# Optimization experiments

Hardware: AMD Instinct MI355X
Metric: run time of the kernel (lower is better)

Reference implementation:

```python
import jax, jax.numpy as jnp
import numpy as np

EMB_DIM = 1024
HEAD_NUM = 16
HEAD_DIM = EMB_DIM // HEAD_NUM
B, S = 2, 2048


def setup_inputs() -> dict:
    key = jax.random.key(0)
    k_x, k_wqkv, k_bqkv, k_wo, k_bo = jax.random.split(key, 5)
    x = jax.random.normal(k_x, (B, S, EMB_DIM), dtype=jnp.float32)
    # nn.Linear default init scale ~ 1/sqrt(fan_in); exact distribution irrelevant for a reference
    lim = 1.0 / np.sqrt(EMB_DIM)
    W_qkv = jax.random.uniform(k_wqkv, (EMB_DIM, 3 * EMB_DIM), jnp.float32, -lim, lim)
    b_qkv = jax.random.uniform(k_bqkv, (3 * EMB_DIM,), jnp.float32, -lim, lim)
    W_o = jax.random.uniform(k_wo, (EMB_DIM, EMB_DIM), jnp.float32, -lim, lim)
    b_o = jax.random.uniform(k_bo, (EMB_DIM,), jnp.float32, -lim, lim)
    mask = jnp.tril(jnp.ones((S, S), dtype=bool))  # causal mask as in casual_mask(seq_len)
    return {"x": x, "W_qkv": W_qkv, "b_qkv": b_qkv, "W_o": W_o, "b_o": b_o, "mask": mask}


def reference(x, W_qkv, b_qkv, W_o, b_o, mask):
    b, s, e = x.shape
    qkv = x @ W_qkv + b_qkv                      # [b, s, 3e]
    q, k, v = qkv[..., :e], qkv[..., e:2 * e], qkv[..., 2 * e:]
    # [b, s, h, d] -> [b, h, s, d]
    q = q.reshape(b, s, HEAD_NUM, HEAD_DIM).transpose(0, 2, 1, 3)
    k = k.reshape(b, s, HEAD_NUM, HEAD_DIM).transpose(0, 2, 1, 3)
    v = v.reshape(b, s, HEAD_NUM, HEAD_DIM).transpose(0, 2, 1, 3)
    scores = jnp.einsum("bhqd,bhkd->bhqk", q, k) / jnp.sqrt(jnp.float32(HEAD_DIM))
    scores = jnp.where(mask, scores, -jnp.inf)   # masked_fill(~mask, -inf)
    probs = jax.nn.softmax(scores, axis=-1)      # dropout is identity in eval mode
    out = jnp.einsum("bhqk,bhkd->bhqd", probs, v)
    out = out.transpose(0, 2, 1, 3).reshape(b, s, e)
    return out @ W_o + b_o
```

## Files before the change

### kernel.cpp

```cpp
#include <hip/hip_runtime.h>


typedef __attribute__((ext_vector_type(8))) short short8;
typedef __attribute__((ext_vector_type(4))) short short4v;
typedef __attribute__((ext_vector_type(4))) float floatx4;

#define NB 2
#define SEQ 2048
#define EMB 1024
#define NH 16
#define HD 64
#define M_ROWS (NB * SEQ)
#define N_QKV (3 * EMB)
#define SLOT_B 16896
#define SLOTS_PER_BH 24

#define GLL(g, l) __builtin_amdgcn_global_load_lds( \
    (const __attribute__((address_space(1))) void*)(g), \
    (__attribute__((address_space(3))) void*)(l), 16, 0, 0)

#if defined(__HIP_DEVICE_COMPILE__)
#define MFMA16K16(A, B, C) __builtin_amdgcn_mfma_f32_16x16x16bf16_1k(A, B, C, 0, 0, 0)
#else
#define MFMA16K16(A, B, C) (C)
#endif

static __device__ __forceinline__ unsigned short f2bf(float f) {
    union { float f; unsigned int u; } v; v.f = f;
    unsigned int r = v.u + 0x7FFFu + ((v.u >> 16) & 1u);
    return (unsigned short)(r >> 16);
}
static __device__ __forceinline__ float bf2f(unsigned short h) {
    union { unsigned int u; float f; } v; v.u = ((unsigned int)h) << 16;
    return v.f;
}

static __device__ __forceinline__ unsigned int cvt_pk_bf16(float lo, float hi) {
#if defined(__HIP_DEVICE_COMPILE__)
    unsigned int r;
    asm("v_cvt_pk_bf16_f32 %0, %1, %2" : "=v"(r) : "v"(lo), "v"(hi));
    return r;
#else
    (void)lo; (void)hi; return 0u;
#endif
}
static __device__ __forceinline__ short4v pack4bf(float a, float b, float c, float d) {
    union { unsigned int u[2]; short4v s; } pu;
    pu.u[0] = cvt_pk_bf16(a, b);
    pu.u[1] = cvt_pk_bf16(c, d);
    return pu.s;
}

__constant__ unsigned char FQT[40] = {
    3,11,14,15,15, 9,12,13,  7,11,14,15, 6, 9,12,13,
    7,11,15, 5, 6,10,13,14, 10, 2, 4, 5, 8,10,13,14,
    0, 1, 4, 8, 8, 9,12,12 };
__constant__ unsigned char FCI[40] = {
    0, 0, 1, 1, 3, 1, 1, 2,  0, 1, 3, 2, 0, 2, 3, 3,
    1, 2, 0, 0, 1, 0, 0, 0,  2, 0, 0, 1, 1, 1, 1, 2,
    0, 0, 1, 0, 2, 0, 0, 2 };

static __device__ __forceinline__ int slot_off(int qt2, int ci) {
    int so = (qt2 < 8) ? (qt2 - 4)
           : (qt2 < 12 ? 4 + (qt2 - 8) * 2 : 12 + (qt2 - 12) * 3);
    return so + (ci - 1);
}

__global__ void prep(const float* __restrict__ x,
                     const float* __restrict__ Wqkv, const float* __restrict__ Wo,
                     unsigned short* __restrict__ x_bf,
                     unsigned short* __restrict__ wqkvT, unsigned short* __restrict__ woT) {
    __shared__ unsigned short tile[32][33];
    int z = blockIdx.z;
    int tx = threadIdx.x, ty = threadIdx.y;
    if (z == 2) {
        int id = ((int)blockIdx.y * 96 + (int)blockIdx.x) * 256 + ty * 32 + tx;
        const int n4 = M_ROWS * EMB / 4;
        for (int i = id; i < n4; i += 96 * 32 * 256) {
            float4 v = ((const float4*)x)[i];
            unsigned long long p = (unsigned long long)f2bf(v.x)
                | ((unsigned long long)f2bf(v.y) << 16)
                | ((unsigned long long)f2bf(v.z) << 32)
                | ((unsigned long long)f2bf(v.w) << 48);
            ((unsigned long long*)x_bf)[i] = p;
        }
        return;
    }
    int C = z ? EMB : N_QKV;
    if ((int)blockIdx.x * 32 >= C) return;
    const float* in = z ? Wo : Wqkv;
    unsigned short* out = z ? woT : wqkvT;
    const int R = EMB;
    int c0 = blockIdx.x * 32, r0 = blockIdx.y * 32;
    #pragma unroll
    for (int j = 0; j < 4; ++j)
        tile[ty + j * 8][tx] = f2bf(in[(size_t)(r0 + ty + j * 8) * C + c0 + tx]);
    __syncthreads();
    #pragma unroll
    for (int j = 0; j < 4; ++j)
        out[(size_t)(c0 + ty + j * 8) * R + r0 + tx] = tile[tx][ty + j * 8];
}

#define CTS 130

__global__ __launch_bounds__(256) void qkv_gemm(
    const unsigned short* __restrict__ A,
    const unsigned short* __restrict__ Bt,
    const float* __restrict__ bias,
    unsigned short* __restrict__ qb, unsigned short* __restrict__ kb,
    unsigned short* __restrict__ vb)
{
    const int K = EMB;
    __shared__ __align__(16) unsigned short smem[128 * CTS];

    int t = threadIdx.x;
    int m0 = blockIdx.y * 128;
    int n0 = blockIdx.x * 128;
    int w = t >> 6, lane = t & 63, quad = lane >> 4, lcol = lane & 15;
    int wr = w >> 1, wc = w & 1;

    floatx4 zero = {0.f, 0.f, 0.f, 0.f};
    floatx4 acc[4][4];
    #pragma unroll
    for (int i = 0; i < 4; ++i)
        #pragma unroll
        for (int j = 0; j < 4; ++j) acc[i][j] = zero;

    const unsigned short* a0 = A  + (size_t)(m0 + (t >> 2)) * K + ((t & 3) << 3);
    const unsigned short* b0 = Bt + (size_t)(n0 + (t >> 2)) * K + ((t & 3) << 3);
    unsigned short* la = &smem[t << 3];

    GLL(a0, la);
    GLL(a0 + 64 * K, la + 2048);
    GLL(b0, la + 4096);
    GLL(b0 + 64 * K, la + 6144);

    for (int k0 = 0; k0 < K; k0 += 32) {
        int cur = (k0 >> 5) & 1, nxt = cur ^ 1;
        __syncthreads();
        if (k0 + 32 < K) {
            GLL(a0 + k0 + 32, la + nxt * 8192);
            GLL(a0 + 64 * K + k0 + 32, la + nxt * 8192 + 2048);
            GLL(b0 + k0 + 32, la + nxt * 8192 + 4096);
            GLL(b0 + 64 * K + k0 + 32, la + nxt * 8192 + 6144);
        }
        const unsigned short* As = &smem[cur * 8192];
        const unsigned short* Bs = As + 4096;
        short8 af[4], bfm[4];
        #pragma unroll
        for (int i = 0; i < 4; ++i)
            af[i] = *(const short8*)(&As[(wr * 64 + i * 16 + lcol) * 32 + quad * 8]);
        #pragma unroll
        for (int j = 0; j < 4; ++j)
            bfm[j] = *(const short8*)(&Bs[(wc * 64 + j * 16 + lcol) * 32 + quad * 8]);
        #pragma unroll
        for (int i = 0; i < 4; ++i)
            #pragma unroll
            for (int j = 0; j < 4; ++j)
                acc[i][j] = __builtin_amdgcn_mfma_f32_16x16x32_bf16(af[i], bfm[j], acc[i][j], 0, 0, 0);
    }

    bool isV = (n0 >= 2 * EMB);
    __syncthreads();
    #pragma unroll
    for (int i = 0; i < 4; ++i) {
        int row0 = wr * 64 + i * 16 + quad * 4;
        #pragma unroll
        for (int j = 0; j < 4; ++j) {
            int col = wc * 64 + j * 16 + lcol;
            float bv = bias[n0 + col];
            #pragma unroll
            for (int r = 0; r < 4; ++r) {
                unsigned short hv = f2bf(acc[i][j][r] + bv);
                if (isV) smem[col * CTS + row0 + r] = hv;
                else     smem[(row0 + r) * CTS + col] = hv;
            }
        }
    }
    __syncthreads();

    int b = m0 >> 11, s0 = m0 & 2047;
    int hbase = (n0 & 1023) >> 6;
    if (!isV) {
        unsigned short* dst = (n0 >= EMB) ? kb : qb;
        #pragma unroll
        for (int it = 0; it < 8; ++it) {
            int job = it * 32 + (t >> 3);
            int tok = job & 127, hh = job >> 7;
            int chunk = t & 7;
            short8 vv = *(const short8*)(&smem[tok * CTS + hh * 64 + chunk * 8]);
            size_t g = ((size_t)((b * NH + hbase + hh) * SEQ + s0 + tok)) * HD + chunk * 8;
            *(short8*)(&dst[g]) = vv;
        }
    } else {
        #pragma unroll
        for (int it = 0; it < 8; ++it) {
            int job = it * 32 + (t >> 3);
            int f = job & 127, half = job >> 7;
            int chunk = (t & 7) + half * 8;
            short8 vv = *(const short8*)(&smem[f * CTS + chunk * 8]);
            int h = hbase + (f >> 6), d = f & 63;
            size_t g = ((size_t)((b * NH + h) * HD + d)) * SEQ + s0 + chunk * 8;
            *(short8*)(&vb[g]) = vv;
        }
    }
}

__global__ __launch_bounds__(256) void attn_fused(
    const unsigned short* __restrict__ Q,
    const unsigned short* __restrict__ Kk,
    const unsigned short* __restrict__ Vt,
    unsigned short* __restrict__ Out,
    unsigned char* __restrict__ Part,
    float* __restrict__ Laux)
{
    __shared__ __align__(16) unsigned short Ks[2][64 * 64];
    __shared__ __align__(16) unsigned short Vs[2][64 * 64];

    int fid = (int)blockIdx.y * 40 + (int)blockIdx.x;
    int bh  = (fid & 7) * 4 + ((fid >> 3) & 3);
    int qq  = fid >> 5;
    int qt2 = FQT[qq];
    int ci  = FCI[qq];
    int nc  = 1 + (qt2 >> 2);
    int nt  = 2 * (qt2 + 1);
    int t0  = (nt * ci) / nc, t1 = (nt * (ci + 1)) / nc;
    int q0  = qt2 * 128;

    int t = threadIdx.x;
    int w = t >> 6, lane = t & 63, quad = lane >> 4, lcol = lane & 15;
    const size_t hoff = (size_t)bh * SEQ * HD;
    const float SC = 0.18033688011112043f;

    short8 aq[2][2];
    #pragma unroll
    for (int g = 0; g < 2; ++g) {
        const unsigned short* qp = Q + hoff
            + (size_t)(q0 + g * 64 + 16 * w + lcol) * HD + quad * 8;
        aq[g][0] = *(const short8*)qp;
        aq[g][1] = *(const short8*)(qp + 32);
    }

    int srow = t >> 3;
    int ss   = (t & 7) ^ (srow & 7);
    const unsigned short* kgl = Kk + hoff + (size_t)srow * HD + ss * 8;
    const unsigned short* vgl = Vt + hoff + (size_t)srow * SEQ + ss * 8;
    unsigned short* kld = &Ks[0][t * 8];
    unsigned short* vld = &Vs[0][t * 8];

    floatx4 zero = {0.f, 0.f, 0.f, 0.f};
    floatx4 O[2][4];
    floatx4 lacc[2];
    #pragma unroll
    for (int g = 0; g < 2; ++g) {
        lacc[g] = zero;
        #pragma unroll
        for (int td = 0; td < 4; ++td) O[g][td] = zero;
    }

    short4v ones4;
    #pragma unroll
    for (int jj = 0; jj < 4; ++jj) ones4[jj] = (short)0x3F80;

    {
        int pb = (t0 & 1) * 4096;
        size_t k0 = (size_t)t0 * 64;
        GLL(kgl + k0 * HD, kld + pb);
        GLL(kgl + (k0 + 32) * HD, kld + pb + 2048);
        GLL(vgl + k0, vld + pb);
        GLL(vgl + (size_t)32 * SEQ + k0, vld + pb + 2048);
    }

    int sx0 = (quad ^ (lcol & 7)) << 3;
    int sx1 = sx0 ^ 32;

    for (int kt = t0; kt < t1; ++kt) {
        int cur = kt & 1, nxt = cur ^ 1;
        __syncthreads();
        if (kt + 1 < t1) {
            size_t k0 = (size_t)(kt + 1) * 64;
            GLL(kgl + k0 * HD, kld + nxt * 4096);
            GLL(kgl + (k0 + 32) * HD, kld + nxt * 4096 + 2048);
            GLL(vgl + k0, vld + nxt * 4096);
            GLL(vgl + (size_t)32 * SEQ + k0, vld + nxt * 4096 + 2048);
        }

        const unsigned short* ksr = &Ks[cur][0];
        const unsigned short* vsr = &Vs[cur][0];
        short8 bk0[4], bk1[4];
        #pragma unroll
        for (int tc = 0; tc < 4; ++tc) {
            int rb = (tc * 16 + lcol) << 6;
            bk0[tc] = *(const short8*)(ksr + rb + sx0);
            bk1[tc] = *(const short8*)(ksr + rb + sx1);
        }

        short4v pk[2][4];
        bool act[2];
        #pragma unroll
        for (int g = 0; g < 2; ++g) {
            const int gb = q0 + g * 64 + 16 * w;
            act[g] = (kt * 64 <= gb + 15);
            if (act[g]) {
                floatx4 sacc[4];
                #pragma unroll
                for (int tc = 0; tc < 4; ++tc) {
                    sacc[tc] = __builtin_amdgcn_mfma_f32_16x16x32_bf16(bk0[tc], aq[g][0], zero, 0, 0, 0);
                    sacc[tc] = __builtin_amdgcn_mfma_f32_16x16x32_bf16(bk1[tc], aq[g][1], sacc[tc], 0, 0, 0);
                }
                if (kt * 64 + 63 > gb) {
                    int qrow = gb + lcol;
                    #pragma unroll
                    for (int tc = 0; tc < 4; ++tc) {
                        float p[4];
                        #pragma unroll
                        for (int r = 0; r < 4; ++r) {
                            float e = __builtin_amdgcn_exp2f(sacc[tc][r] * SC);
                            p[r] = (kt * 64 + tc * 16 + quad * 4 + r > qrow) ? 0.f : e;
                        }
                        pk[g][tc] = pack4bf(p[0], p[1], p[2], p[3]);
                    }
                } else {
                    #pragma unroll
                    for (int tc = 0; tc < 4; ++tc) {
                        pk[g][tc] = pack4bf(
                            __builtin_amdgcn_exp2f(sacc[tc][0] * SC),
                            __builtin_amdgcn_exp2f(sacc[tc][1] * SC),
                            __builtin_amdgcn_exp2f(sacc[tc][2] * SC),
                            __builtin_amdgcn_exp2f(sacc[tc][3] * SC));
                    }
                }
            }
        }

        #pragma unroll
        for (int td = 0; td < 4; ++td) {
            short4v va[4];
            #pragma unroll
            for (int tc = 0; tc < 4; ++tc) {
                int seg = ((tc << 1) + (quad >> 1)) ^ (lcol & 7);
                va[tc] = *(const short4v*)(vsr + ((td * 16 + lcol) << 6) + (seg << 3) + ((quad & 1) << 2));
            }
            if (act[0]) {
                #pragma unroll
                for (int tc = 0; tc < 4; ++tc)
                    O[0][td] = MFMA16K16(va[tc], pk[0][tc], O[0][td]);
            }
            if (act[1]) {
                #pragma unroll
                for (int tc = 0; tc < 4; ++tc)
                    O[1][td] = MFMA16K16(va[tc], pk[1][tc], O[1][td]);
            }
        }
        #pragma unroll
        for (int g = 0; g < 2; ++g) {
            if (act[g]) {
                #pragma unroll
                for (int tc = 0; tc < 4; ++tc)
                    lacc[g] = MFMA16K16(ones4, pk[g][tc], lacc[g]);
            }
        }
    }

    if (nc == 1) {
        int b = bh >> 4, h = bh & 15;
        #pragma unroll
        for (int g = 0; g < 2; ++g) {
            int qrow = q0 + g * 64 + 16 * w + lcol;
            float inv = 1.0f / lacc[g][0];
            size_t obase = ((size_t)b * SEQ + qrow) * EMB + (size_t)h * HD + quad * 4;
            #pragma unroll
            for (int td = 0; td < 4; ++td) {
                short4v ov;
                #pragma unroll
                for (int r = 0; r < 4; ++r) ov[r] = (short)f2bf(O[g][td][r] * inv);
                *(short4v*)(&Out[obase + td * 16]) = ov;
            }
        }
    } else if (ci == 0) {
        int b = bh >> 4, h = bh & 15;
        float* lrow = Laux + ((size_t)bh * 12 + (qt2 - 4)) * 128;
        #pragma unroll
        for (int g = 0; g < 2; ++g) {
            int ql = g * 64 + 16 * w + lcol;
            int qrow = q0 + ql;
            size_t obase = ((size_t)b * SEQ + qrow) * EMB + (size_t)h * HD + quad * 4;
            #pragma unroll
            for (int td = 0; td < 4; ++td) {
                short4v ov;
                #pragma unroll
                for (int r = 0; r < 4; ++r) ov[r] = (short)f2bf(O[g][td][r]);
                *(short4v*)(&Out[obase + td * 16]) = ov;
            }
            if (quad == 0) lrow[ql] = lacc[g][0];
        }
    } else {
        unsigned char* sp = Part
            + (size_t)(bh * SLOTS_PER_BH + slot_off(qt2, ci)) * SLOT_B;
        unsigned short* sO = (unsigned short*)sp;
        float* sL = (float*)(sp + 16384);
        #pragma unroll
        for (int g = 0; g < 2; ++g) {
            int ql = g * 64 + 16 * w + lcol;
            #pragma unroll
            for (int td = 0; td < 4; ++td) {
                short4v ov;
                #pragma unroll
                for (int r = 0; r < 4; ++r) ov[r] = (short)f2bf(O[g][td][r]);
                *(short4v*)(&sO[ql * 64 + td * 16 + quad * 4]) = ov;
            }
            if (quad == 0) sL[ql] = lacc[g][0];
        }
    }
}

__global__ __launch_bounds__(256) void attn_combine(
    const unsigned char* __restrict__ Part, const float* __restrict__ Laux,
    unsigned short* __restrict__ Out)
{
    int qt2 = 4 + (int)blockIdx.x;
    int bh = blockIdx.y;
    int nc = 1 + (qt2 >> 2);
    const unsigned char* base = Part
        + (size_t)(bh * SLOTS_PER_BH + slot_off(qt2, 1)) * SLOT_B;
    const float* lrow = Laux + ((size_t)bh * 12 + (qt2 - 4)) * 128;
    int b = bh >> 4, h = bh & 15;
    size_t obase = ((size_t)b * SEQ + qt2 * 128) * EMB + (size_t)h * HD;
    int t = threadIdx.x;
    #pragma unroll
    for (int it = 0; it < 4; ++it) {
        int job = it * 256 + t;
        int row = job >> 3, c8 = (job & 7) * 8;
        unsigned short* op = &Out[obase + (size_t)row * EMB + c8];
        float acc8[8];
        short8 v0 = *(const short8*)op;
        #pragma unroll
        for (int e = 0; e < 8; ++e) acc8[e] = bf2f((unsigned short)v0[e]);
        float lsum = lrow[row];
        for (int k = 1; k < nc; ++k) {
            const unsigned char* sp = base + (size_t)(k - 1) * SLOT_B;
            const unsigned short* sO = (const unsigned short*)sp;
            const float* sL = (const float*)(sp + 16384);
            short8 vv = *(const short8*)(&sO[row * 64 + c8]);
            #pragma unroll
            for (int e = 0; e < 8; ++e) acc8[e] += bf2f((unsigned short)vv[e]);
            lsum += sL[row];
        }
        float inv = 1.0f / lsum;
        short8 ov;
        #pragma unroll
        for (int e = 0; e < 8; ++e) ov[e] = (short)f2bf(acc8[e] * inv);
        *(short8*)op = ov;
    }
}

__global__ __launch_bounds__(256) void oproj_gemm(
    const unsigned short* __restrict__ A,
    const unsigned short* __restrict__ Bt,
    const float* __restrict__ bias,
    float* __restrict__ Cout)
{
    const int K = EMB;
    __shared__ __align__(16) unsigned short smem[2 * 8192];
    int t = threadIdx.x;
    int m0 = blockIdx.y * 128;
    int n0 = blockIdx.x * 128;
    int w = t >> 6, lane = t & 63, quad = lane >> 4, lcol = lane & 15;
    int wr = w >> 1, wc = w & 1;

    floatx4 zero = {0.f, 0.f, 0.f, 0.f};
    floatx4 acc[4][4];
    #pragma unroll
    for (int i = 0; i < 4; ++i)
        #pragma unroll
        for (int j = 0; j < 4; ++j) acc[i][j] = zero;

    const unsigned short* a0 = A  + (size_t)(m0 + (t >> 2)) * K + ((t & 3) << 3);
    const unsigned short* b0 = Bt + (size_t)(n0 + (t >> 2)) * K + ((t & 3) << 3);
    unsigned short* la = &smem[t << 3];

    GLL(a0, la);
    GLL(a0 + 64 * K, la + 2048);
    GLL(b0, la + 4096);
    GLL(b0 + 64 * K, la + 6144);

    for (int k0 = 0; k0 < K; k0 += 32) {
        int cur = (k0 >> 5) & 1, nxt = cur ^ 1;
        __syncthreads();
        if (k0 + 32 < K) {
            GLL(a0 + k0 + 32, la + nxt * 8192);
            GLL(a0 + 64 * K + k0 + 32, la + nxt * 8192 + 2048);
            GLL(b0 + k0 + 32, la + nxt * 8192 + 4096);
            GLL(b0 + 64 * K + k0 + 32, la + nxt * 8192 + 6144);
        }
        const unsigned short* As = &smem[cur * 8192];
        const unsigned short* Bs = As + 4096;
        short8 af[4], bfm[4];
        #pragma unroll
        for (int i = 0; i < 4; ++i)
            af[i] = *(const short8*)(&As[(wr * 64 + i * 16 + lcol) * 32 + quad * 8]);
        #pragma unroll
        for (int j = 0; j < 4; ++j)
            bfm[j] = *(const short8*)(&Bs[(wc * 64 + j * 16 + lcol) * 32 + quad * 8]);
        #pragma unroll
        for (int i = 0; i < 4; ++i)
            #pragma unroll
            for (int j = 0; j < 4; ++j)
                acc[i][j] = __builtin_amdgcn_mfma_f32_16x16x32_bf16(af[i], bfm[j], acc[i][j], 0, 0, 0);
    }

    #pragma unroll
    for (int i = 0; i < 4; ++i) {
        int m = m0 + wr * 64 + i * 16 + quad * 4;
        #pragma unroll
        for (int j = 0; j < 4; ++j) {
            int n = n0 + wc * 64 + j * 16 + lcol;
            float bv = bias[n];
            #pragma unroll
            for (int r = 0; r < 4; ++r)
                Cout[(size_t)(m + r) * EMB + n] = acc[i][j][r] + bv;
        }
    }
}

extern "C" void kernel_launch(void* const* d_in, const int* in_sizes, int n_in,
                              void* d_out, int out_size, void* d_ws, size_t ws_size,
                              hipStream_t stream) {
    (void)in_sizes; (void)n_in; (void)out_size; (void)ws_size;
    char* ws = (char*)d_ws;
    const size_t OFF_X     = 0;
    const size_t OFF_WQKVT = OFF_X     + (size_t)M_ROWS * EMB * 2;
    const size_t OFF_WOT   = OFF_WQKVT + (size_t)N_QKV * EMB * 2;
    const size_t OFF_Q     = OFF_WOT   + (size_t)EMB * EMB * 2;
    const size_t OFF_K     = OFF_Q     + (size_t)M_ROWS * EMB * 2;
    const size_t OFF_V     = OFF_K     + (size_t)M_ROWS * EMB * 2;
    const size_t OFF_ATTN  = OFF_V     + (size_t)M_ROWS * EMB * 2;
    const size_t OFF_PART  = OFF_X;
    const size_t OFF_LAUX  = OFF_PART + (size_t)32 * SLOTS_PER_BH * SLOT_B;

    const float* x    = (const float*)d_in[0];
    const float* Wqkv = (const float*)d_in[1];
    const float* bqkv = (const float*)d_in[2];
    const float* Wo   = (const float*)d_in[3];
    const float* bo   = (const float*)d_in[4];

    unsigned short* x_bf  = (unsigned short*)(ws + OFF_X);
    unsigned short* wqkvT = (unsigned short*)(ws + OFF_WQKVT);
    unsigned short* woT   = (unsigned short*)(ws + OFF_WOT);
    unsigned short* qb    = (unsigned short*)(ws + OFF_Q);
    unsigned short* kb    = (unsigned short*)(ws + OFF_K);
    unsigned short* vb    = (unsigned short*)(ws + OFF_V);
    unsigned short* attn  = (unsigned short*)(ws + OFF_ATTN);
    unsigned char*  part  = (unsigned char*)(ws + OFF_PART);
    float*          laux  = (float*)(ws + OFF_LAUX);

    prep<<<dim3(96, 32, 3), dim3(32, 8), 0, stream>>>(x, Wqkv, Wo, x_bf, wqkvT, woT);

    qkv_gemm<<<dim3(N_QKV / 128, M_ROWS / 128), 256, 0, stream>>>(x_bf, wqkvT, bqkv, qb, kb, vb);
    attn_fused<<<dim3(40, NB * NH), 256, 0, stream>>>(qb, kb, vb, attn, part, laux);
    attn_combine<<<dim3(12, NB * NH), 256, 0, stream>>>(part, laux, attn);
    oproj_gemm<<<dim3(EMB / 128, M_ROWS / 128), 256, 0, stream>>>(attn, woT, bo, (float*)d_out);
}
```

Before: 201.0 us.

## Use 256-row query tiles with 512 threads and triple-buffered K/V pipeline

Doubles the attention query tile to 256 rows and the block to 512 threads (8 waves), so each K/V tile loaded into shared memory is reused by twice as many query rows. The split-K work table, partial slots and combine kernel are rebuilt for the coarser tiles. The K/V double buffer becomes a three-stage buffer with explicit vmcnt waits, raw barriers and prefetching two tiles ahead. K fragment loads are moved under the causal-activity check so inactive groups skip them. The larger blocks give fewer blocks and coarser load balance, and the hand-written waitcnt counts must match the number of outstanding loads exactly.

```diff
diff --git a/kernel.cpp b/kernel.cpp
--- a/kernel.cpp
+++ b/kernel.cpp
@@ -12,8 +12,8 @@
 #define HD 64
 #define M_ROWS (NB * SEQ)
 #define N_QKV (3 * EMB)
-#define SLOT_B 16896
-#define SLOTS_PER_BH 24
+#define SLOT_B 33792
+#define SLOTS_PER_BH 12
 
 #define GLL(g, l) __builtin_amdgcn_global_load_lds( \
     (const __attribute__((address_space(1))) void*)(g), \
@@ -51,18 +51,14 @@
     return pu.s;
 }
 
-__constant__ unsigned char FQT[40] = {
-    3,11,14,15,15, 9,12,13,  7,11,14,15, 6, 9,12,13,
-    7,11,15, 5, 6,10,13,14, 10, 2, 4, 5, 8,10,13,14,
-    0, 1, 4, 8, 8, 9,12,12 };
-__constant__ unsigned char FCI[40] = {
-    0, 0, 1, 1, 3, 1, 1, 2,  0, 1, 3, 2, 0, 2, 3, 3,
-    1, 2, 0, 0, 1, 0, 0, 0,  2, 0, 0, 1, 1, 1, 1, 2,
-    0, 0, 1, 0, 2, 0, 0, 2 };
-
-static __device__ __forceinline__ int slot_off(int qt2, int ci) {
-    int so = (qt2 < 8) ? (qt2 - 4)
-           : (qt2 < 12 ? 4 + (qt2 - 8) * 2 : 12 + (qt2 - 12) * 3);
+__constant__ unsigned char FQT[20] = {
+    1,3,3,5,5,5,7,7,7,7, 4,4,6,6,6,6, 2,2,4, 0 };
+__constant__ unsigned char FCI[20] = {
+    0,0,1,0,1,2,0,1,2,3, 1,2,0,1,2,3, 0,1,0, 0 };
+
+static __device__ __forceinline__ int slot_off(int qt3, int ci) {
+    int so = (qt3 < 4) ? (qt3 - 2)
+           : (qt3 < 6 ? 2 + (qt3 - 4) * 2 : 6 + (qt3 - 6) * 3);
     return so + (ci - 1);
 }
 
@@ -206,7 +202,7 @@
     }
 }
 
-__global__ __launch_bounds__(256) void attn_fused(
+__global__ __launch_bounds__(512) void attn_fused(
     const unsigned short* __restrict__ Q,
     const unsigned short* __restrict__ Kk,
     const unsigned short* __restrict__ Vt,
@@ -214,18 +210,18 @@
     unsigned char* __restrict__ Part,
     float* __restrict__ Laux)
 {
-    __shared__ __align__(16) unsigned short Ks[2][64 * 64];
-    __shared__ __align__(16) unsigned short Vs[2][64 * 64];
-
-    int fid = (int)blockIdx.y * 40 + (int)blockIdx.x;
+    __shared__ __align__(16) unsigned short Ks[3][64 * 64];
+    __shared__ __align__(16) unsigned short Vs[3][64 * 64];
+
+    int fid = (int)blockIdx.y * 20 + (int)blockIdx.x;
     int bh  = (fid & 7) * 4 + ((fid >> 3) & 3);
     int qq  = fid >> 5;
-    int qt2 = FQT[qq];
+    int qt3 = FQT[qq];
     int ci  = FCI[qq];
-    int nc  = 1 + (qt2 >> 2);
-    int nt  = 2 * (qt2 + 1);
+    int nc  = (qt3 + 2) >> 1;
+    int nt  = 4 * (qt3 + 1);
     int t0  = (nt * ci) / nc, t1 = (nt * (ci + 1)) / nc;
-    int q0  = qt2 * 128;
+    int q0  = qt3 * 256;
 
     int t = threadIdx.x;
     int w = t >> 6, lane = t & 63, quad = lane >> 4, lcol = lane & 15;
@@ -236,10 +232,11 @@
     #pragma unroll
     for (int g = 0; g < 2; ++g) {
         const unsigned short* qp = Q + hoff
-            + (size_t)(q0 + g * 64 + 16 * w + lcol) * HD + quad * 8;
+            + (size_t)(q0 + g * 128 + 16 * w + lcol) * HD + quad * 8;
         aq[g][0] = *(const short8*)qp;
         aq[g][1] = *(const short8*)(qp + 32);
     }
+    asm volatile("s_waitcnt vmcnt(0)" ::: "memory");
 
     int srow = t >> 3;
     int ss   = (t & 7) ^ (srow & 7);
@@ -248,6 +245,12 @@
     unsigned short* kld = &Ks[0][t * 8];
     unsigned short* vld = &Vs[0][t * 8];
 
+#define STAGE(kt_, buf_) do { \
+        size_t kk_ = (size_t)(kt_) * 64; \
+        GLL(kgl + kk_ * HD, kld + (buf_) * 4096); \
+        GLL(vgl + kk_,      vld + (buf_) * 4096); \
+    } while (0)
+
     floatx4 zero = {0.f, 0.f, 0.f, 0.f};
     floatx4 O[2][4];
     floatx4 lacc[2];
@@ -262,46 +265,36 @@
     #pragma unroll
     for (int jj = 0; jj < 4; ++jj) ones4[jj] = (short)0x3F80;
 
-    {
-        int pb = (t0 & 1) * 4096;
-        size_t k0 = (size_t)t0 * 64;
-        GLL(kgl + k0 * HD, kld + pb);
-        GLL(kgl + (k0 + 32) * HD, kld + pb + 2048);
-        GLL(vgl + k0, vld + pb);
-        GLL(vgl + (size_t)32 * SEQ + k0, vld + pb + 2048);
-    }
+    STAGE(t0, t0 % 3);
+    if (t0 + 1 < t1) STAGE(t0 + 1, (t0 + 1) % 3);
 
     int sx0 = (quad ^ (lcol & 7)) << 3;
     int sx1 = sx0 ^ 32;
 
     for (int kt = t0; kt < t1; ++kt) {
-        int cur = kt & 1, nxt = cur ^ 1;
-        __syncthreads();
-        if (kt + 1 < t1) {
-            size_t k0 = (size_t)(kt + 1) * 64;
-            GLL(kgl + k0 * HD, kld + nxt * 4096);
-            GLL(kgl + (k0 + 32) * HD, kld + nxt * 4096 + 2048);
-            GLL(vgl + k0, vld + nxt * 4096);
-            GLL(vgl + (size_t)32 * SEQ + k0, vld + nxt * 4096 + 2048);
-        }
-
-        const unsigned short* ksr = &Ks[cur][0];
-        const unsigned short* vsr = &Vs[cur][0];
-        short8 bk0[4], bk1[4];
-        #pragma unroll
-        for (int tc = 0; tc < 4; ++tc) {
-            int rb = (tc * 16 + lcol) << 6;
-            bk0[tc] = *(const short8*)(ksr + rb + sx0);
-            bk1[tc] = *(const short8*)(ksr + rb + sx1);
-        }
+        if (kt + 1 < t1) asm volatile("s_waitcnt vmcnt(2)" ::: "memory");
+        else             asm volatile("s_waitcnt vmcnt(0)" ::: "memory");
+        __builtin_amdgcn_s_barrier();
+        __builtin_amdgcn_sched_barrier(0);
+
+        int b3 = kt % 3;
+        const unsigned short* ksr = &Ks[b3][0];
+        const unsigned short* vsr = &Vs[b3][0];
 
         short4v pk[2][4];
         bool act[2];
         #pragma unroll
         for (int g = 0; g < 2; ++g) {
-            const int gb = q0 + g * 64 + 16 * w;
+            const int gb = q0 + g * 128 + 16 * w;
             act[g] = (kt * 64 <= gb + 15);
             if (act[g]) {
+                short8 bk0[4], bk1[4];
+                #pragma unroll
+                for (int tc = 0; tc < 4; ++tc) {
+                    int rb = (tc * 16 + lcol) << 6;
+                    bk0[tc] = *(const short8*)(ksr + rb + sx0);
+                    bk1[tc] = *(const short8*)(ksr + rb + sx1);
+                }
                 floatx4 sacc[4];
                 #pragma unroll
                 for (int tc = 0; tc < 4; ++tc) {
@@ -333,20 +326,33 @@
             }
         }
 
-        #pragma unroll
-        for (int td = 0; td < 4; ++td) {
-            short4v va[4];
-            #pragma unroll
-            for (int tc = 0; tc < 4; ++tc) {
-                int seg = ((tc << 1) + (quad >> 1)) ^ (lcol & 7);
-                va[tc] = *(const short4v*)(vsr + ((td * 16 + lcol) << 6) + (seg << 3) + ((quad & 1) << 2));
-            }
-            if (act[0]) {
+        if (act[0]) {
+            #pragma unroll
+            for (int td = 0; td < 4; ++td) {
+                short4v va[4];
+                #pragma unroll
+                for (int tc = 0; tc < 4; ++tc) {
+                    int seg = ((tc << 1) + (quad >> 1)) ^ (lcol & 7);
+                    va[tc] = *(const short4v*)(vsr + ((td * 16 + lcol) << 6) + (seg << 3) + ((quad & 1) << 2));
+                }
                 #pragma unroll
                 for (int tc = 0; tc < 4; ++tc)
                     O[0][td] = MFMA16K16(va[tc], pk[0][tc], O[0][td]);
-            }
-            if (act[1]) {
+                if (act[1]) {
+                    #pragma unroll
+                    for (int tc = 0; tc < 4; ++tc)
+                        O[1][td] = MFMA16K16(va[tc], pk[1][tc], O[1][td]);
+                }
+            }
+        } else if (act[1]) {
+            #pragma unroll
+            for (int td = 0; td < 4; ++td) {
+                short4v va[4];
+                #pragma unroll
+                for (int tc = 0; tc < 4; ++tc) {
+                    int seg = ((tc << 1) + (quad >> 1)) ^ (lcol & 7);
+                    va[tc] = *(const short4v*)(vsr + ((td * 16 + lcol) << 6) + (seg << 3) + ((quad & 1) << 2));
+                }
                 #pragma unroll
                 for (int tc = 0; tc < 4; ++tc)
                     O[1][td] = MFMA16K16(va[tc], pk[1][tc], O[1][td]);
@@ -360,13 +366,17 @@
                     lacc[g] = MFMA16K16(ones4, pk[g][tc], lacc[g]);
             }
         }
-    }
+
+        __builtin_amdgcn_sched_barrier(0);
+        if (kt + 2 < t1) STAGE(kt + 2, (kt + 2) % 3);
+    }
+#undef STAGE
 
     if (nc == 1) {
         int b = bh >> 4, h = bh & 15;
         #pragma unroll
         for (int g = 0; g < 2; ++g) {
-            int qrow = q0 + g * 64 + 16 * w + lcol;
+            int qrow = q0 + g * 128 + 16 * w + lcol;
             float inv = 1.0f / lacc[g][0];
             size_t obase = ((size_t)b * SEQ + qrow) * EMB + (size_t)h * HD + quad * 4;
             #pragma unroll
@@ -379,10 +389,10 @@
         }
     } else if (ci == 0) {
         int b = bh >> 4, h = bh & 15;
-        float* lrow = Laux + ((size_t)bh * 12 + (qt2 - 4)) * 128;
+        float* lrow = Laux + ((size_t)bh * 6 + (qt3 - 2)) * 256;
         #pragma unroll
         for (int g = 0; g < 2; ++g) {
-            int ql = g * 64 + 16 * w + lcol;
+            int ql = g * 128 + 16 * w + lcol;
             int qrow = q0 + ql;
             size_t obase = ((size_t)b * SEQ + qrow) * EMB + (size_t)h * HD + quad * 4;
             #pragma unroll
@@ -396,12 +406,12 @@
         }
     } else {
         unsigned char* sp = Part
-            + (size_t)(bh * SLOTS_PER_BH + slot_off(qt2, ci)) * SLOT_B;
+            + (size_t)(bh * SLOTS_PER_BH + slot_off(qt3, ci)) * SLOT_B;
         unsigned short* sO = (unsigned short*)sp;
-        float* sL = (float*)(sp + 16384);
+        float* sL = (float*)(sp + 32768);
         #pragma unroll
         for (int g = 0; g < 2; ++g) {
-            int ql = g * 64 + 16 * w + lcol;
+            int ql = g * 128 + 16 * w + lcol;
             #pragma unroll
             for (int td = 0; td < 4; ++td) {
                 short4v ov;
@@ -418,17 +428,17 @@
     const unsigned char* __restrict__ Part, const float* __restrict__ Laux,
     unsigned short* __restrict__ Out)
 {
-    int qt2 = 4 + (int)blockIdx.x;
+    int qt3 = 2 + (int)blockIdx.x;
     int bh = blockIdx.y;
-    int nc = 1 + (qt2 >> 2);
+    int nc = (qt3 + 2) >> 1;
     const unsigned char* base = Part
-        + (size_t)(bh * SLOTS_PER_BH + slot_off(qt2, 1)) * SLOT_B;
-    const float* lrow = Laux + ((size_t)bh * 12 + (qt2 - 4)) * 128;
+        + (size_t)(bh * SLOTS_PER_BH + slot_off(qt3, 1)) * SLOT_B;
+    const float* lrow = Laux + ((size_t)bh * 6 + (qt3 - 2)) * 256;
     int b = bh >> 4, h = bh & 15;
-    size_t obase = ((size_t)b * SEQ + qt2 * 128) * EMB + (size_t)h * HD;
+    size_t obase = ((size_t)b * SEQ + qt3 * 256) * EMB + (size_t)h * HD;
     int t = threadIdx.x;
     #pragma unroll
-    for (int it = 0; it < 4; ++it) {
+    for (int it = 0; it < 8; ++it) {
         int job = it * 256 + t;
         int row = job >> 3, c8 = (job & 7) * 8;
         unsigned short* op = &Out[obase + (size_t)row * EMB + c8];
@@ -440,7 +450,7 @@
         for (int k = 1; k < nc; ++k) {
             const unsigned char* sp = base + (size_t)(k - 1) * SLOT_B;
             const unsigned short* sO = (const unsigned short*)sp;
-            const float* sL = (const float*)(sp + 16384);
+            const float* sL = (const float*)(sp + 32768);
             short8 vv = *(const short8*)(&sO[row * 64 + c8]);
             #pragma unroll
             for (int e = 0; e < 8; ++e) acc8[e] += bf2f((unsigned short)vv[e]);
@@ -557,7 +567,7 @@
     prep<<<dim3(96, 32, 3), dim3(32, 8), 0, stream>>>(x, Wqkv, Wo, x_bf, wqkvT, woT);
 
     qkv_gemm<<<dim3(N_QKV / 128, M_ROWS / 128), 256, 0, stream>>>(x_bf, wqkvT, bqkv, qb, kb, vb);
-    attn_fused<<<dim3(40, NB * NH), 256, 0, stream>>>(qb, kb, vb, attn, part, laux);
-    attn_combine<<<dim3(12, NB * NH), 256, 0, stream>>>(part, laux, attn);
+    attn_fused<<<dim3(20, NB * NH), 512, 0, stream>>>(qb, kb, vb, attn, part, laux);
+    attn_combine<<<dim3(6, NB * NH), 256, 0, stream>>>(part, laux, attn);
     oproj_gemm<<<dim3(EMB / 128, M_ROWS / 128), 256, 0, stream>>>(attn, woT, bo, (float*)d_out);
 }
```

After: 198.1 us. Within noise of the previous version (-1.4%).
